# Optimization experiments

Hardware: AMD Instinct MI355X
Metric: run time of the kernel (lower is better)

Reference implementation:

```python
import jax, jax.numpy as jnp
import numpy as np

B = 64; H = 56; W = 56; C = 96; WS = 7; SHIFT = 3; NH = 3
N = WS * WS          # 49 tokens per window
NW = (H // WS) * (W // WS)  # 64 windows per image
HD = C // NH
MLP_H = 4 * C


def _rel_index():
    coords = np.stack(np.meshgrid(np.arange(WS), np.arange(WS), indexing='ij')).reshape(2, -1)
    rel = (coords[:, :, None] - coords[:, None, :]).transpose(1, 2, 0)
    rel[..., 0] += WS - 1
    rel[..., 1] += WS - 1
    rel[..., 0] *= 2 * WS - 1
    return rel.sum(-1)  # [N, N] int


def _attn_mask():
    img = np.zeros((H, W))
    cnt = 0
    sls = (slice(0, -WS), slice(-WS, -SHIFT), slice(-SHIFT, None))
    for hs in sls:
        for ws_ in sls:
            img[hs, ws_] = cnt
            cnt += 1
    mw = img.reshape(H // WS, WS, W // WS, WS).transpose(0, 2, 1, 3).reshape(-1, N)
    diff = mw[:, None, :] - mw[:, :, None]
    return np.where(diff != 0, -100.0, 0.0).astype(np.float32)  # [NW, N, N]


REL_IDX = jnp.asarray(_rel_index())
MASK = jnp.asarray(_attn_mask())


def _ln(x, g, b):
    mu = x.mean(-1, keepdims=True)
    var = ((x - mu) ** 2).mean(-1, keepdims=True)
    return (x - mu) * jax.lax.rsqrt(var + 1e-5) * g + b


def setup_inputs() -> dict:
    key = jax.random.key(0)
    ks = jax.random.split(key, 8)
    s = 0.02
    return {
        'x': jax.random.normal(ks[0], (B, H * W, C), jnp.float32),
        'norm1_g': jnp.ones((C,), jnp.float32),
        'norm1_b': jnp.zeros((C,), jnp.float32),
        'qkv_w': jax.random.normal(ks[1], (C, 3 * C), jnp.float32) * s,
        'qkv_b': jnp.zeros((3 * C,), jnp.float32),
        'proj_w': jax.random.normal(ks[2], (C, C), jnp.float32) * s,
        'proj_b': jnp.zeros((C,), jnp.float32),
        'rpb_table': jax.random.normal(ks[3], ((2 * WS - 1) ** 2, NH), jnp.float32) * s,
        'norm2_g': jnp.ones((C,), jnp.float32),
        'norm2_b': jnp.zeros((C,), jnp.float32),
        'fc1_w': jax.random.normal(ks[4], (C, MLP_H), jnp.float32) * s,
        'fc1_b': jnp.zeros((MLP_H,), jnp.float32),
        'fc2_w': jax.random.normal(ks[5], (MLP_H, C), jnp.float32) * s,
        'fc2_b': jnp.zeros((C,), jnp.float32),
    }


def reference(x, norm1_g, norm1_b, qkv_w, qkv_b, proj_w, proj_b, rpb_table,
              norm2_g, norm2_b, fc1_w, fc1_b, fc2_w, fc2_b):
    Bx = x.shape[0]
    shortcut = x
    h = _ln(x, norm1_g, norm1_b).reshape(Bx, H, W, C)
    # cyclic shift
    h = jnp.roll(h, (-SHIFT, -SHIFT), axis=(1, 2))
    # window partition -> [B*NW, N, C]
    win = h.reshape(Bx, H // WS, WS, W // WS, WS, C).transpose(0, 1, 3, 2, 4, 5).reshape(-1, N, C)
    B_ = win.shape[0]
    # qkv projection
    qkv = (win @ qkv_w + qkv_b).reshape(B_, N, 3, NH, HD).transpose(2, 0, 3, 1, 4)
    q, k, v = qkv[0], qkv[1], qkv[2]  # [B_, NH, N, HD]
    scale = HD ** -0.5
    attn = jnp.einsum('bhnd,bhmd->bhnm', q * scale, k)  # [B_, NH, N, N]
    bias = rpb_table[REL_IDX.reshape(-1)].reshape(N, N, NH).transpose(2, 0, 1)
    attn = attn + bias[None]
    # shifted-window mask
    attn = attn.reshape(Bx, NW, NH, N, N) + MASK[None, :, None]
    attn = jax.nn.softmax(attn.reshape(B_, NH, N, N), axis=-1)
    out = jnp.einsum('bhnm,bhmd->bnhd', attn, v).reshape(B_, N, C)
    out = out @ proj_w + proj_b
    # window reverse + reverse shift
    out = out.reshape(Bx, H // WS, W // WS, WS, WS, C).transpose(0, 1, 3, 2, 4, 5).reshape(Bx, H, W, C)
    out = jnp.roll(out, (SHIFT, SHIFT), axis=(1, 2)).reshape(Bx, H * W, C)
    x = shortcut + out
    # MLP
    h2 = _ln(x, norm2_g, norm2_b)
    h2 = jax.nn.gelu(h2 @ fc1_w + fc1_b, approximate=False) @ fc2_w + fc2_b
    return x + h2
```

## Files before the change

### kernel.cpp

```cpp
#include <hip/hip_runtime.h>
#include <hip/hip_bf16.h>
#include <math.h>

#define BB    64
#define HH    56
#define WW_   56
#define CC    96
#define WS    7
#define SHIFT 3
#define NHD   3
#define NT    49
#define NWIN  64
#define HD    32
#define MLPH  384
#define HWTOK (HH*WW_)
#define NTOK  (BB*HWTOK)
#define NWTOT (BB*NWIN)

#define IMG_S 10240
#define N_IMG 12
#define WS_NEED (16 + N_IMG*IMG_S*2)

typedef __attribute__((ext_vector_type(8))) short short8;
typedef __attribute__((ext_vector_type(4))) short short4v;
typedef __attribute__((ext_vector_type(4))) float floatx4;

__device__ __forceinline__ float b2fs(short s) {
    union { unsigned int u; float f; } cv;
    cv.u = ((unsigned int)(unsigned short)s) << 16;
    return cv.f;
}
__device__ __forceinline__ short f2b(float f) {
    union { __hip_bfloat16 h; short s; } cv;
    cv.h = __float2bfloat16(f);
    return cv.s;
}
__device__ __forceinline__ float ldv(const void* p, size_t i, bool bf) {
    return bf ? b2fs(((const short*)p)[i]) : ((const float*)p)[i];
}
__device__ __forceinline__ void stv(void* p, size_t i, bool bf, float v) {
    if (bf) ((short*)p)[i] = f2b(v);
    else    ((float*)p)[i] = v;
}
#define MFMA16(a,b,c) __builtin_amdgcn_mfma_f32_16x16x32_bf16((a),(b),(c),0,0,0)

__device__ __forceinline__ float gelu_f(float v) {
    float z  = v * 0.70710678118654752f;
    float az = fabsf(z);
    float t  = __fdividef(1.0f, fmaf(0.3275911f, az, 1.0f));
    float p  = fmaf(fmaf(fmaf(fmaf(1.061405429f, t, -1.453152027f), t,
                   1.421413741f), t, -0.284496736f), t, 0.254829592f) * t;
    float e  = __expf(-az*az);
    float er = fmaf(-p, e, 1.0f);
    er = (z < 0.f) ? -er : er;
    return 0.5f * v * (1.0f + er);
}

__global__ void dtype_probe(const void* __restrict__ n1g, int* __restrict__ flag) {
    if (threadIdx.x == 0) {
        float f = ((const float*)n1g)[0];
        *flag = (f == 1.0f) ? 0 : 1;
    }
}

__global__ void prep_kernel(
    const void* __restrict__ qkv_w, const void* __restrict__ proj_w,
    const void* __restrict__ fc1_w, const void* __restrict__ fc2_w,
    short* __restrict__ wimg, const int* __restrict__ flag)
{
    const bool bf = (*flag != 0);
    int idx = blockIdx.x * 256 + threadIdx.x;
    if (idx >= N_IMG*IMG_S) return;
    int img = idx / IMG_S, r = idx - img*IMG_S;
    short v = 0;
    if (r < 96*104) {
        int nc = r / 104, k = r - nc*104;
        if (k < 96) {
            float f;
            if (img < 3)       f = ldv(qkv_w, (size_t)k*(3*CC) + (nc>>5)*CC + img*HD + (nc&31), bf);
            else if (img == 3) f = ldv(proj_w, (size_t)k*CC + nc, bf);
            else if (img < 8)  f = ldv(fc1_w, (size_t)k*MLPH + (img-4)*96 + nc, bf);
            else               f = ldv(fc2_w, (size_t)((img-8)*96 + k)*CC + nc, bf);
            v = f2b(f);
        }
    }
    wimg[idx] = v;
}

__global__ __launch_bounds__(256, 4) void attn_pre2(
    const void* __restrict__ x,
    const void* __restrict__ n1g, const void* __restrict__ n1b,
    const void* __restrict__ qkv_b, const void* __restrict__ rpb,
    const void* __restrict__ proj_b,
    void* __restrict__ out, const int* __restrict__ flag,
    const short* __restrict__ wimg)
{
    __shared__ __attribute__((aligned(16))) short lx[64*104];
    __shared__ __attribute__((aligned(16))) short lqk[64*72];
    __shared__ __attribute__((aligned(16))) short lv[32*72];
    __shared__ __attribute__((aligned(16))) short lsm[64*72];
    __shared__ float lmu[64], lrs[64];
    __shared__ float lg[CC], lb[CC];
    short* lctx = lx;

    const bool bf = (*flag != 0);
    const int win = blockIdx.x;
    const int b   = win >> 6;
    const int wr  = win & 63;
    const int wh  = wr >> 3, ww = wr & 7;
    const int tid = threadIdx.x;
    const int lane = tid & 63;
    const int wv  = tid >> 6;
    const int c   = lane & 15;
    const int q   = lane >> 4;

    if (tid < CC) { lg[tid] = ldv(n1g, tid, bf); lb[tid] = ldv(n1b, tid, bf); }

    if (!bf) {
        const float* xf = (const float*)x;
        for (int idx = tid; idx < NT*24; idx += 256) {
            int n = idx / 24, c4 = idx - n*24;
            int i = n / WS, j = n - i*WS;
            int hg = wh*WS + i + SHIFT; if (hg >= HH)  hg -= HH;
            int wg = ww*WS + j + SHIFT; if (wg >= WW_) wg -= WW_;
            size_t t = (size_t)(b*HWTOK + hg*WW_ + wg);
            floatx4 v = *(const floatx4*)&xf[t*CC + c4*4];
            short4v s;
            s[0] = f2b(v[0]); s[1] = f2b(v[1]); s[2] = f2b(v[2]); s[3] = f2b(v[3]);
            *(short4v*)&lx[n*104 + c4*4] = s;
        }
    } else {
        for (int idx = tid; idx < NT*CC; idx += 256) {
            int n = idx / CC, cc_ = idx - n*CC;
            int i = n / WS, j = n - i*WS;
            int hg = wh*WS + i + SHIFT; if (hg >= HH)  hg -= HH;
            int wg = ww*WS + j + SHIFT; if (wg >= WW_) wg -= WW_;
            size_t t = (size_t)(b*HWTOK + hg*WW_ + wg);
            lx[n*104 + cc_] = f2b(ldv(x, t*CC + cc_, bf));
        }
    }
    for (int idx = tid; idx < 15*13; idx += 256) {
        int n = NT + idx/13, c8 = idx - (idx/13)*13;
        *(short8*)&lx[n*104 + c8*8] = (short8)0;
    }
    __syncthreads();

    {
        int t = tid >> 2, p = tid & 3;
        float s = 0.f, ss = 0.f;
        #pragma unroll
        for (int i = 0; i < 24; ++i) {
            float v = b2fs(lx[t*104 + p*24 + i]); s += v; ss += v*v;
        }
        s += __shfl_xor(s, 1); ss += __shfl_xor(ss, 1);
        s += __shfl_xor(s, 2); ss += __shfl_xor(ss, 2);
        if (p == 0) {
            float mu = s * (1.f/CC);
            float var = ss * (1.f/CC) - mu*mu;
            lmu[t] = mu; lrs[t] = rsqrtf(var + 1e-5f);
        }
    }
    __syncthreads();

    short8 af[3];
    #pragma unroll
    for (int kt = 0; kt < 3; ++kt) {
        int row = wv*16 + c;
        short8 raw = *(const short8*)&lx[row*104 + kt*32 + q*8];
        float mu = lmu[row], rs = lrs[row];
        short8 a;
        #pragma unroll
        for (int e = 0; e < 8; ++e) {
            int k = kt*32 + q*8 + e;
            a[e] = f2b((b2fs(raw[e]) - mu)*rs*lg[k] + lb[k]);
        }
        af[kt] = a;
    }

    const float scale = 0.17677669529663687f;

    for (int h = 0; h < NHD; ++h) {
        const short* bimg = wimg + h*IMG_S;

        floatx4 acc[6];
        #pragma unroll
        for (int nt = 0; nt < 6; ++nt) acc[nt] = (floatx4)0.f;
        #pragma unroll
        for (int kt = 0; kt < 3; ++kt) {
            #pragma unroll
            for (int nt = 0; nt < 6; ++nt) {
                short8 bfr = *(const short8*)&bimg[(nt*16 + c)*104 + kt*32 + q*8];
                acc[nt] = MFMA16(af[kt], bfr, acc[nt]);
            }
        }
        #pragma unroll
        for (int nt = 0; nt < 6; ++nt) {
            int ncol = nt*16 + c;
            int part = ncol >> 5, d = ncol & 31;
            float bias = ldv(qkv_b, part*CC + h*HD + d, bf);
            #pragma unroll
            for (int r = 0; r < 4; ++r) {
                int trow = wv*16 + q*4 + r;
                float v = acc[nt][r] + bias;
                if (part < 2) lqk[trow*72 + part*32 + d] = f2b(v);
                else          lv[d*72 + trow]            = f2b(v);
            }
        }
        __syncthreads();

        short8 aq = *(const short8*)&lqk[(wv*16 + c)*72 + q*8];
        floatx4 sv[4];
        #pragma unroll
        for (int nt = 0; nt < 4; ++nt) {
            short8 bk = *(const short8*)&lqk[(nt*16 + c)*72 + 32 + q*8];
            sv[nt] = MFMA16(aq, bk, (floatx4)0.f);
        }

        int ikA[4], jkA[4], rkA[4], tkA[4];
        #pragma unroll
        for (int nt = 0; nt < 4; ++nt) {
            int tk = nt*16 + c; tkA[nt] = tk;
            int ik = tk / 7, jk = tk - ik*7;
            ikA[nt] = ik; jkA[nt] = jk;
            int rh = (wh == 7) ? (ik < 4 ? 1 : 2) : 0;
            int rw = (ww == 7) ? (jk < 4 ? 1 : 2) : 0;
            rkA[nt] = rh*3 + rw;
        }
        #pragma unroll
        for (int r = 0; r < 4; ++r) {
            int tq = wv*16 + q*4 + r;
            int iq = tq / 7, jq = tq - iq*7;
            int rhq = (wh == 7) ? (iq < 4 ? 1 : 2) : 0;
            int rwq = (ww == 7) ? (jq < 4 ? 1 : 2) : 0;
            int rq = rhq*3 + rwq;
            float vals[4], mx = -1e30f;
            #pragma unroll
            for (int nt = 0; nt < 4; ++nt) {
                float v;
                if (tkA[nt] < NT) {
                    int rel = (iq - ikA[nt] + 6)*13 + (jq - jkA[nt] + 6);
                    rel = rel < 0 ? 0 : (rel > 168 ? 168 : rel);
                    v = sv[nt][r]*scale + ldv(rpb, rel*NHD + h, bf);
                    if (rkA[nt] != rq) v -= 100.f;
                } else v = -1e30f;
                vals[nt] = v; mx = fmaxf(mx, v);
            }
            mx = fmaxf(mx, __shfl_xor(mx, 1));
            mx = fmaxf(mx, __shfl_xor(mx, 2));
            mx = fmaxf(mx, __shfl_xor(mx, 4));
            mx = fmaxf(mx, __shfl_xor(mx, 8));
            float sum = 0.f;
            #pragma unroll
            for (int nt = 0; nt < 4; ++nt) { vals[nt] = __expf(vals[nt] - mx); sum += vals[nt]; }
            sum += __shfl_xor(sum, 1);
            sum += __shfl_xor(sum, 2);
            sum += __shfl_xor(sum, 4);
            sum += __shfl_xor(sum, 8);
            float inv = 1.f / sum;
            #pragma unroll
            for (int nt = 0; nt < 4; ++nt)
                lsm[(wv*16 + q*4 + r)*72 + nt*16 + c] = f2b(vals[nt]*inv);
        }
        floatx4 ov[2] = {(floatx4)0.f, (floatx4)0.f};
        #pragma unroll
        for (int kt = 0; kt < 2; ++kt) {
            short8 ap = *(const short8*)&lsm[(wv*16 + c)*72 + kt*32 + q*8];
            #pragma unroll
            for (int nt = 0; nt < 2; ++nt) {
                short8 bv = *(const short8*)&lv[(nt*16 + c)*72 + kt*32 + q*8];
                ov[nt] = MFMA16(ap, bv, ov[nt]);
            }
        }
        #pragma unroll
        for (int nt = 0; nt < 2; ++nt)
            #pragma unroll
            for (int r = 0; r < 4; ++r)
                lctx[(wv*16 + q*4 + r)*104 + h*HD + nt*16 + c] = f2b(ov[nt][r]);
        if (h < NHD-1) __syncthreads();
    }

    const short* pimg = wimg + 3*IMG_S;
    floatx4 po[6];
    #pragma unroll
    for (int nt = 0; nt < 6; ++nt) po[nt] = (floatx4)0.f;
    #pragma unroll
    for (int kt = 0; kt < 3; ++kt) {
        short8 ac = *(const short8*)&lctx[(wv*16 + c)*104 + kt*32 + q*8];
        #pragma unroll
        for (int nt = 0; nt < 6; ++nt) {
            short8 bp = *(const short8*)&pimg[(nt*16 + c)*104 + kt*32 + q*8];
            po[nt] = MFMA16(ac, bp, po[nt]);
        }
    }
    float pbv[6];
    #pragma unroll
    for (int nt = 0; nt < 6; ++nt) pbv[nt] = ldv(proj_b, nt*16 + c, bf);
    #pragma unroll
    for (int r = 0; r < 4; ++r) {
        int n = wv*16 + q*4 + r;
        if (n < NT) {
            int i = n / WS, j = n - i*WS;
            int hg = wh*WS + i + SHIFT; if (hg >= HH)  hg -= HH;
            int wg = ww*WS + j + SHIFT; if (wg >= WW_) wg -= WW_;
            size_t gbase = (size_t)(b*HWTOK + hg*WW_ + wg)*CC;
            #pragma unroll
            for (int nt = 0; nt < 6; ++nt) {
                size_t gi = gbase + nt*16 + c;
                stv(out, gi, bf, po[nt][r] + pbv[nt] + ldv(x, gi, bf));
            }
        }
    }
}

__global__ __launch_bounds__(256, 2) void mlp_x2(
    void* __restrict__ out,
    const void* __restrict__ n2g, const void* __restrict__ n2b,
    const void* __restrict__ fc1_b, const void* __restrict__ fc2_b,
    const int* __restrict__ flag, const short* __restrict__ wimg)
{
    __shared__ __attribute__((aligned(16))) short lx1[128*104];
    __shared__ float lmu[128], lrs[128];
    __shared__ float lg[CC], lb[CC];
    short* lh = lx1;

    const bool bf = (*flag != 0);
    const int t0  = blockIdx.x * 128;
    const int tid = threadIdx.x;
    const int lane = tid & 63;
    const int wv  = tid >> 6;
    const int rb  = wv * 32;
    const int c   = lane & 15;
    const int q   = lane >> 4;

    if (tid < CC) { lg[tid] = ldv(n2g, tid, bf); lb[tid] = ldv(n2b, tid, bf); }

    if (!bf) {
        const float* of = (const float*)out;
        for (int idx = lane; idx < 32*24; idx += 64) {
            int n = idx / 24, c4 = idx - n*24;
            floatx4 v = *(const floatx4*)&of[(size_t)(t0+rb+n)*CC + c4*4];
            short4v s;
            s[0] = f2b(v[0]); s[1] = f2b(v[1]); s[2] = f2b(v[2]); s[3] = f2b(v[3]);
            *(short4v*)&lx1[(rb+n)*104 + c4*4] = s;
        }
    } else {
        for (int idx = lane; idx < 32*CC; idx += 64) {
            int n = idx / CC, cc_ = idx - n*CC;
            lx1[(rb+n)*104 + cc_] = f2b(ldv(out, (size_t)(t0+rb+n)*CC + cc_, bf));
        }
    }

    {
        int tr = rb + (lane >> 1), p = lane & 1;
        float s = 0.f, ss = 0.f;
        #pragma unroll
        for (int i = 0; i < 48; ++i) {
            float v = b2fs(lx1[tr*104 + p*48 + i]); s += v; ss += v*v;
        }
        s += __shfl_xor(s, 1); ss += __shfl_xor(ss, 1);
        if (p == 0) {
            float mu = s * (1.f/CC);
            float var = ss * (1.f/CC) - mu*mu;
            lmu[tr] = mu; lrs[tr] = rsqrtf(var + 1e-5f);
        }
    }
    __syncthreads();

    short8 af[2][3];
    #pragma unroll
    for (int tt = 0; tt < 2; ++tt) {
        #pragma unroll
        for (int kt = 0; kt < 3; ++kt) {
            int row = rb + tt*16 + c;
            short8 raw = *(const short8*)&lx1[row*104 + kt*32 + q*8];
            float mu = lmu[row], rs = lrs[row];
            short8 a;
            #pragma unroll
            for (int e = 0; e < 8; ++e) {
                int k = kt*32 + q*8 + e;
                a[e] = f2b((b2fs(raw[e]) - mu)*rs*lg[k] + lb[k]);
            }
            af[tt][kt] = a;
        }
    }

    floatx4 acc2[2][6];
    #pragma unroll
    for (int tt = 0; tt < 2; ++tt)
        #pragma unroll
        for (int nt = 0; nt < 6; ++nt) acc2[tt][nt] = (floatx4)0.f;

    for (int qh = 0; qh < 4; ++qh) {
        const short* b1 = wimg + (4+qh)*IMG_S;
        #pragma unroll
        for (int nh = 0; nh < 2; ++nh) {
            floatx4 a1[2][3];
            #pragma unroll
            for (int tt = 0; tt < 2; ++tt)
                #pragma unroll
                for (int nt2 = 0; nt2 < 3; ++nt2) a1[tt][nt2] = (floatx4)0.f;
            #pragma unroll
            for (int kt = 0; kt < 3; ++kt) {
                #pragma unroll
                for (int nt2 = 0; nt2 < 3; ++nt2) {
                    int nt = nh*3 + nt2;
                    short8 bfr = *(const short8*)&b1[(nt*16 + c)*104 + kt*32 + q*8];
                    a1[0][nt2] = MFMA16(af[0][kt], bfr, a1[0][nt2]);
                    a1[1][nt2] = MFMA16(af[1][kt], bfr, a1[1][nt2]);
                }
            }
            #pragma unroll
            for (int nt2 = 0; nt2 < 3; ++nt2) {
                int nl = (nh*3 + nt2)*16 + c;
                float bias = ldv(fc1_b, qh*96 + nl, bf);
                #pragma unroll
                for (int tt = 0; tt < 2; ++tt) {
                    #pragma unroll
                    for (int r = 0; r < 4; ++r) {
                        float v = a1[tt][nt2][r] + bias;
                        lh[(rb + tt*16 + q*4 + r)*104 + nl] = f2b(gelu_f(v));
                    }
                }
            }
        }
        __syncthreads();

        const short* b2 = wimg + (8+qh)*IMG_S;
        #pragma unroll
        for (int kt = 0; kt < 3; ++kt) {
            short8 ah0 = *(const short8*)&lh[(rb + c)*104 + kt*32 + q*8];
            short8 ah1 = *(const short8*)&lh[(rb + 16 + c)*104 + kt*32 + q*8];
            #pragma unroll
            for (int nt = 0; nt < 6; ++nt) {
                short8 bw = *(const short8*)&b2[(nt*16 + c)*104 + kt*32 + q*8];
                acc2[0][nt] = MFMA16(ah0, bw, acc2[0][nt]);
                acc2[1][nt] = MFMA16(ah1, bw, acc2[1][nt]);
            }
        }
    }

    float b2v[6];
    #pragma unroll
    for (int nt = 0; nt < 6; ++nt) b2v[nt] = ldv(fc2_b, nt*16 + c, bf);
    #pragma unroll
    for (int tt = 0; tt < 2; ++tt) {
        #pragma unroll
        for (int r = 0; r < 4; ++r) {
            int row = rb + tt*16 + q*4 + r;
            size_t gbase = (size_t)(t0 + row)*CC;
            #pragma unroll
            for (int nt = 0; nt < 6; ++nt) {
                size_t gi = gbase + nt*16 + c;
                stv(out, gi, bf, acc2[tt][nt][r] + b2v[nt] + ldv(out, gi, bf));
            }
        }
    }
}

__global__ __launch_bounds__(256, 2) void attn_old(
    const void* __restrict__ x,
    const void* __restrict__ n1g, const void* __restrict__ n1b,
    const void* __restrict__ qkv_w, const void* __restrict__ qkv_b,
    const void* __restrict__ rpb,
    const void* __restrict__ proj_w, const void* __restrict__ proj_b,
    void* __restrict__ out, const int* __restrict__ flag)
{
    __shared__ __attribute__((aligned(16))) short lx[64*104];
    __shared__ __attribute__((aligned(16))) short lwb[96*104];
    __shared__ __attribute__((aligned(16))) short lqk[64*72];
    __shared__ __attribute__((aligned(16))) short lv[32*72];
    __shared__ __attribute__((aligned(16))) short lctx[64*104];
    __shared__ float lmu[64], lrs[64];
    __shared__ float lg[CC], lb[CC];
    short* lsm = lwb;

    const bool bf = (*flag != 0);
    const int win = blockIdx.x;
    const int b   = win >> 6;
    const int wr  = win & 63;
    const int wh  = wr >> 3, ww = wr & 7;
    const int tid = threadIdx.x;
    const int lane = tid & 63;
    const int wv  = tid >> 6;
    const int c   = lane & 15;
    const int q   = lane >> 4;

    if (tid < CC) { lg[tid] = ldv(n1g, tid, bf); lb[tid] = ldv(n1b, tid, bf); }

    for (int idx = tid; idx < NT*CC; idx += 256) {
        int n = idx / CC, cc_ = idx - n*CC;
        int i = n / WS, j = n - i*WS;
        int hg = wh*WS + i + SHIFT; if (hg >= HH)  hg -= HH;
        int wg = ww*WS + j + SHIFT; if (wg >= WW_) wg -= WW_;
        size_t t = (size_t)(b*HWTOK + hg*WW_ + wg);
        lx[n*104 + cc_] = f2b(ldv(x, t*CC + cc_, bf));
    }
    for (int idx = tid; idx < 15*CC; idx += 256) {
        int n = NT + idx/CC, cc_ = idx % CC;
        lx[n*104 + cc_] = 0;
    }
    __syncthreads();

    {
        int t = tid >> 2, p = tid & 3;
        float s = 0.f, ss = 0.f;
        #pragma unroll
        for (int i = 0; i < 24; ++i) {
            float v = b2fs(lx[t*104 + p*24 + i]); s += v; ss += v*v;
        }
        s += __shfl_xor(s, 1); ss += __shfl_xor(ss, 1);
        s += __shfl_xor(s, 2); ss += __shfl_xor(ss, 2);
        if (p == 0) {
            float mu = s * (1.f/CC);
            float var = ss * (1.f/CC) - mu*mu;
            lmu[t] = mu; lrs[t] = rsqrtf(var + 1e-5f);
        }
    }
    __syncthreads();
    for (int idx = tid; idx < NT*CC; idx += 256) {
        int n = idx / CC, cc_ = idx - n*CC;
        float v = b2fs(lx[n*104 + cc_]);
        lx[n*104 + cc_] = f2b((v - lmu[n]) * lrs[n] * lg[cc_] + lb[cc_]);
    }
    __syncthreads();

    const float scale = 0.17677669529663687f;

    for (int h = 0; h < NHD; ++h) {
        for (int idx = tid; idx < 96*96; idx += 256) {
            int k = idx / 96, nc = idx - (idx/96)*96;
            int part = nc >> 5, d = nc & 31;
            lwb[nc*104 + k] = f2b(ldv(qkv_w, (size_t)k*(3*CC) + part*CC + h*HD + d, bf));
        }
        __syncthreads();

        floatx4 acc[6];
        #pragma unroll
        for (int nt = 0; nt < 6; ++nt) acc[nt] = (floatx4)0.f;
        #pragma unroll
        for (int kt = 0; kt < 3; ++kt) {
            short8 af = *(const short8*)&lx[(wv*16 + c)*104 + kt*32 + q*8];
            #pragma unroll
            for (int nt = 0; nt < 6; ++nt) {
                short8 bfr = *(const short8*)&lwb[(nt*16 + c)*104 + kt*32 + q*8];
                acc[nt] = MFMA16(af, bfr, acc[nt]);
            }
        }
        #pragma unroll
        for (int nt = 0; nt < 6; ++nt) {
            int ncol = nt*16 + c;
            int part = ncol >> 5, d = ncol & 31;
            float bias = ldv(qkv_b, part*CC + h*HD + d, bf);
            #pragma unroll
            for (int r = 0; r < 4; ++r) {
                int trow = wv*16 + q*4 + r;
                float v = acc[nt][r] + bias;
                if (part < 2) lqk[trow*72 + part*32 + d] = f2b(v);
                else          lv[d*72 + trow]            = f2b(v);
            }
        }
        __syncthreads();

        short8 aq = *(const short8*)&lqk[(wv*16 + c)*72 + q*8];
        floatx4 sv[4];
        #pragma unroll
        for (int nt = 0; nt < 4; ++nt) {
            short8 bk = *(const short8*)&lqk[(nt*16 + c)*72 + 32 + q*8];
            sv[nt] = MFMA16(aq, bk, (floatx4)0.f);
        }

        int ikA[4], jkA[4], rkA[4], tkA[4];
        #pragma unroll
        for (int nt = 0; nt < 4; ++nt) {
            int tk = nt*16 + c; tkA[nt] = tk;
            int ik = tk / 7, jk = tk - ik*7;
            ikA[nt] = ik; jkA[nt] = jk;
            int rh = (wh == 7) ? (ik < 4 ? 1 : 2) : 0;
            int rw = (ww == 7) ? (jk < 4 ? 1 : 2) : 0;
            rkA[nt] = rh*3 + rw;
        }
        #pragma unroll
        for (int r = 0; r < 4; ++r) {
            int tq = wv*16 + q*4 + r;
            int iq = tq / 7, jq = tq - iq*7;
            int rhq = (wh == 7) ? (iq < 4 ? 1 : 2) : 0;
            int rwq = (ww == 7) ? (jq < 4 ? 1 : 2) : 0;
            int rq = rhq*3 + rwq;
            float vals[4], mx = -1e30f;
            #pragma unroll
            for (int nt = 0; nt < 4; ++nt) {
                float v;
                if (tkA[nt] < NT) {
                    int rel = (iq - ikA[nt] + 6)*13 + (jq - jkA[nt] + 6);
                    rel = rel < 0 ? 0 : (rel > 168 ? 168 : rel);
                    v = sv[nt][r]*scale + ldv(rpb, rel*NHD + h, bf);
                    if (rkA[nt] != rq) v -= 100.f;
                } else v = -1e30f;
                vals[nt] = v; mx = fmaxf(mx, v);
            }
            mx = fmaxf(mx, __shfl_xor(mx, 1));
            mx = fmaxf(mx, __shfl_xor(mx, 2));
            mx = fmaxf(mx, __shfl_xor(mx, 4));
            mx = fmaxf(mx, __shfl_xor(mx, 8));
            float sum = 0.f;
            #pragma unroll
            for (int nt = 0; nt < 4; ++nt) { vals[nt] = __expf(vals[nt] - mx); sum += vals[nt]; }
            sum += __shfl_xor(sum, 1);
            sum += __shfl_xor(sum, 2);
            sum += __shfl_xor(sum, 4);
            sum += __shfl_xor(sum, 8);
            float inv = 1.f / sum;
            #pragma unroll
            for (int nt = 0; nt < 4; ++nt)
                lsm[(wv*16 + q*4 + r)*72 + nt*16 + c] = f2b(vals[nt]*inv);
        }
        floatx4 ov[2] = {(floatx4)0.f, (floatx4)0.f};
        #pragma unroll
        for (int kt = 0; kt < 2; ++kt) {
            short8 ap = *(const short8*)&lsm[(wv*16 + c)*72 + kt*32 + q*8];
            #pragma unroll
            for (int nt = 0; nt < 2; ++nt) {
                short8 bv = *(const short8*)&lv[(nt*16 + c)*72 + kt*32 + q*8];
                ov[nt] = MFMA16(ap, bv, ov[nt]);
            }
        }
        #pragma unroll
        for (int nt = 0; nt < 2; ++nt)
            #pragma unroll
            for (int r = 0; r < 4; ++r)
                lctx[(wv*16 + q*4 + r)*104 + h*HD + nt*16 + c] = f2b(ov[nt][r]);
        __syncthreads();
    }

    for (int idx = tid; idx < 96*96; idx += 256) {
        int k = idx / 96, nc = idx - (idx/96)*96;
        lwb[nc*104 + k] = f2b(ldv(proj_w, (size_t)k*CC + nc, bf));
    }
    __syncthreads();

    floatx4 po[6];
    #pragma unroll
    for (int nt = 0; nt < 6; ++nt) po[nt] = (floatx4)0.f;
    #pragma unroll
    for (int kt = 0; kt < 3; ++kt) {
        short8 ac = *(const short8*)&lctx[(wv*16 + c)*104 + kt*32 + q*8];
        #pragma unroll
        for (int nt = 0; nt < 6; ++nt) {
            short8 bp = *(const short8*)&lwb[(nt*16 + c)*104 + kt*32 + q*8];
            po[nt] = MFMA16(ac, bp, po[nt]);
        }
    }
    #pragma unroll
    for (int nt = 0; nt < 6; ++nt) {
        int ncol = nt*16 + c;
        float bias = ldv(proj_b, ncol, bf);
        #pragma unroll
        for (int r = 0; r < 4; ++r) {
            int n = wv*16 + q*4 + r;
            if (n < NT) {
                int i = n / WS, j = n - i*WS;
                int hg = wh*WS + i + SHIFT; if (hg >= HH)  hg -= HH;
                int wg = ww*WS + j + SHIFT; if (wg >= WW_) wg -= WW_;
                size_t t = (size_t)(b*HWTOK + hg*WW_ + wg);
                stv(out, t*CC + ncol, bf, po[nt][r] + bias + ldv(x, t*CC + ncol, bf));
            }
        }
    }
}

__global__ __launch_bounds__(256, 3) void mlp_old(
    void* __restrict__ out,
    const void* __restrict__ n2g, const void* __restrict__ n2b,
    const void* __restrict__ fc1_w, const void* __restrict__ fc1_b,
    const void* __restrict__ fc2_w, const void* __restrict__ fc2_b,
    const int* __restrict__ flag)
{
    __shared__ __attribute__((aligned(16))) short lx1[64*104];
    __shared__ __attribute__((aligned(16))) short lh[64*104];
    __shared__ __attribute__((aligned(16))) short lw[96*104];
    __shared__ float lmu[64], lrs[64];
    __shared__ float lg[CC], lb[CC];

    const bool bf = (*flag != 0);
    const int t0  = blockIdx.x * 64;
    const int tid = threadIdx.x;
    const int lane = tid & 63;
    const int wv  = tid >> 6;
    const int c   = lane & 15;
    const int q   = lane >> 4;

    if (tid < CC) { lg[tid] = ldv(n2g, tid, bf); lb[tid] = ldv(n2b, tid, bf); }
    for (int idx = tid; idx < 64*CC; idx += 256) {
        int n = idx / CC, cc_ = idx - n*CC;
        lx1[n*104 + cc_] = f2b(ldv(out, (size_t)(t0+n)*CC + cc_, bf));
    }
    __syncthreads();

    {
        int t = tid >> 2, p = tid & 3;
        float s = 0.f, ss = 0.f;
        #pragma unroll
        for (int i = 0; i < 24; ++i) {
            float v = b2fs(lx1[t*104 + p*24 + i]); s += v; ss += v*v;
        }
        s += __shfl_xor(s, 1); ss += __shfl_xor(ss, 1);
        s += __shfl_xor(s, 2); ss += __shfl_xor(ss, 2);
        if (p == 0) {
            float mu = s * (1.f/CC);
            float var = ss * (1.f/CC) - mu*mu;
            lmu[t] = mu; lrs[t] = rsqrtf(var + 1e-5f);
        }
    }
    __syncthreads();

    short8 af[3];
    #pragma unroll
    for (int kt = 0; kt < 3; ++kt) {
        int row = wv*16 + c;
        short8 raw = *(const short8*)&lx1[row*104 + kt*32 + q*8];
        float mu = lmu[row], rs = lrs[row];
        short8 a;
        #pragma unroll
        for (int e = 0; e < 8; ++e) {
            int k = kt*32 + q*8 + e;
            a[e] = f2b((b2fs(raw[e]) - mu)*rs*lg[k] + lb[k]);
        }
        af[kt] = a;
    }

    floatx4 acc2[6];
    #pragma unroll
    for (int nt = 0; nt < 6; ++nt) acc2[nt] = (floatx4)0.f;

    for (int qh = 0; qh < 4; ++qh) {
        for (int idx = tid; idx < 96*96; idx += 256) {
            int k = idx / 96, nl = idx - (idx/96)*96;
            lw[nl*104 + k] = f2b(ldv(fc1_w, (size_t)k*MLPH + qh*96 + nl, bf));
        }
        __syncthreads();

        floatx4 a1[6];
        #pragma unroll
        for (int nt = 0; nt < 6; ++nt) a1[nt] = (floatx4)0.f;
        #pragma unroll
        for (int kt = 0; kt < 3; ++kt) {
            #pragma unroll
            for (int nt = 0; nt < 6; ++nt) {
                short8 bfr = *(const short8*)&lw[(nt*16 + c)*104 + kt*32 + q*8];
                a1[nt] = MFMA16(af[kt], bfr, a1[nt]);
            }
        }
        #pragma unroll
        for (int nt = 0; nt < 6; ++nt) {
            int nl = nt*16 + c;
            float bias = ldv(fc1_b, qh*96 + nl, bf);
            #pragma unroll
            for (int r = 0; r < 4; ++r) {
                float v = a1[nt][r] + bias;
                float g = 0.5f*v*(1.f + erff(v*0.70710678118654752f));
                lh[(wv*16 + q*4 + r)*104 + nl] = f2b(g);
            }
        }
        __syncthreads();

        for (int idx = tid; idx < 96*96; idx += 256) {
            int kl = idx / 96, n = idx - (idx/96)*96;
            lw[n*104 + kl] = f2b(ldv(fc2_w, (size_t)(qh*96 + kl)*CC + n, bf));
        }
        __syncthreads();

        #pragma unroll
        for (int kt = 0; kt < 3; ++kt) {
            short8 ah = *(const short8*)&lh[(wv*16 + c)*104 + kt*32 + q*8];
            #pragma unroll
            for (int nt = 0; nt < 6; ++nt) {
                short8 bw = *(const short8*)&lw[(nt*16 + c)*104 + kt*32 + q*8];
                acc2[nt] = MFMA16(ah, bw, acc2[nt]);
            }
        }
        __syncthreads();
    }

    #pragma unroll
    for (int nt = 0; nt < 6; ++nt) {
        int ncol = nt*16 + c;
        float bias = ldv(fc2_b, ncol, bf);
        #pragma unroll
        for (int r = 0; r < 4; ++r) {
            int row = wv*16 + q*4 + r;
            size_t gi = (size_t)(t0 + row)*CC + ncol;
            stv(out, gi, bf, acc2[nt][r] + bias + ldv(out, gi, bf));
        }
    }
}

__global__ void mfma_probe(void* __restrict__ out, const int* __restrict__ flag) {
    __shared__ float A[16*32];
    __shared__ float Bm[32*16];
    __shared__ __attribute__((aligned(16))) short As[16*104];
    __shared__ int lf1[64], lf2[64];

    const bool bfm = (*flag != 0);
    const int tid = threadIdx.x;
    for (int i = tid; i < 16*32; i += 64) {
        int m = i >> 5, k = i & 31;
        A[i] = (float)((m*7 + k*3) % 11 - 5) * 0.125f;
    }
    for (int i = tid; i < 32*16; i += 64) {
        int k = i >> 4, n = i & 15;
        Bm[i] = (float)((k*5 + n*2) % 13 - 6) * 0.0625f;
    }
    __syncthreads();
    for (int i = tid; i < 16*32; i += 64) {
        int m = i >> 5, k = i & 31;
        As[m*104 + k] = f2b(A[i]);
    }
    __syncthreads();

    const int c = tid & 15, q = tid >> 4;
    short8 a, b;
    #pragma unroll
    for (int j = 0; j < 8; ++j) {
        a[j] = f2b(A[c*32 + q*8 + j]);
        b[j] = f2b(Bm[(q*8 + j)*16 + c]);
    }
    short8 av = *(const short8*)&As[c*104 + q*8];
    int f2 = 0;
    #pragma unroll
    for (int j = 0; j < 8; ++j) if (av[j] != a[j]) f2 = 1;

    floatx4 acc = (floatx4)0.f;
    acc = MFMA16(a, b, acc);
    int f1 = 0;
    #pragma unroll
    for (int r = 0; r < 4; ++r) {
        float ref = 0.f;
        for (int k = 0; k < 32; ++k)
            ref += b2fs(f2b(A[(q*4 + r)*32 + k])) * b2fs(f2b(Bm[k*16 + c]));
        float d = fabsf(acc[r] - ref);
        if (!(d <= 0.02f)) f1 = 1;
    }
    lf1[tid] = f1; lf2[tid] = f2;
    __syncthreads();

    if (tid == 0) {
        int any1 = 0, any2 = 0;
        for (int i = 0; i < 64; ++i) { any1 |= lf1[i]; any2 |= lf2[i]; }
        float pert = any1 ? 0.06f : 0.f;
        float tiny = 0.f;
        if (any2) {
            float s = 1.0001f;
            for (int i = 0; i < 400000; ++i) s = s * 0.9999999f + 1e-9f;
            tiny = s * 1e-38f;
        }
        stv(out, 0, bfm, ldv(out, 0, bfm) + pert + tiny);
    }
}

extern "C" void kernel_launch(void* const* d_in, const int* in_sizes, int n_in,
                              void* d_out, int out_size, void* d_ws, size_t ws_size,
                              hipStream_t stream) {
    const void* x      = d_in[0];
    const void* n1g    = d_in[1];
    const void* n1b    = d_in[2];
    const void* qkv_w  = d_in[3];
    const void* qkv_b  = d_in[4];
    const void* proj_w = d_in[5];
    const void* proj_b = d_in[6];
    const void* rpb    = d_in[7];
    const void* n2g    = d_in[8];
    const void* n2b    = d_in[9];
    const void* fc1_w  = d_in[10];
    const void* fc1_b  = d_in[11];
    const void* fc2_w  = d_in[12];
    const void* fc2_b  = d_in[13];
    int* flag = (int*)d_ws;

    hipLaunchKernelGGL(dtype_probe, dim3(1), dim3(64), 0, stream, n1g, flag);

    if (ws_size >= (size_t)WS_NEED) {
        short* wimg = (short*)((char*)d_ws + 16);
        hipLaunchKernelGGL(prep_kernel, dim3((N_IMG*IMG_S + 255)/256), dim3(256), 0, stream,
                           qkv_w, proj_w, fc1_w, fc2_w, wimg, flag);
        hipLaunchKernelGGL(attn_pre2, dim3(NWTOT), dim3(256), 0, stream,
                           x, n1g, n1b, qkv_b, rpb, proj_b, d_out, flag, wimg);
        hipLaunchKernelGGL(mlp_x2, dim3(NTOK/128), dim3(256), 0, stream,
                           d_out, n2g, n2b, fc1_b, fc2_b, flag, wimg);
    } else {
        hipLaunchKernelGGL(attn_old, dim3(NWTOT), dim3(256), 0, stream,
                           x, n1g, n1b, qkv_w, qkv_b, rpb, proj_w, proj_b, d_out, flag);
        hipLaunchKernelGGL(mlp_old, dim3(NTOK/64), dim3(256), 0, stream,
                           d_out, n2g, n2b, fc1_w, fc1_b, fc2_w, fc2_b, flag);
    }
    hipLaunchKernelGGL(mfma_probe, dim3(1), dim3(64), 0, stream, d_out, flag);
}
```

Measured before the change: 489.3 us.

## Process each attention window with two waves, each covering 32 rows

The window attention kernel now runs 128 threads (two waves) per window instead of four, with each wave handling two 16-row tiles. B-fragments loaded from the weight image are shared across the two tiles, and per-wave copies of the LayerNorm parameters plus wave-local row ownership remove two block barriers. The softmax buffer is aliased onto the QK buffer, with an added barrier, to cut LDS use. The aim is less redundant weight loading and fewer syncs, at the cost of more registers per thread and possibly less latency hiding per window.

```diff
diff --git a/kernel.cpp b/kernel.cpp
--- a/kernel.cpp
+++ b/kernel.cpp
@@ -87,7 +87,7 @@
     wimg[idx] = v;
 }
 
-__global__ __launch_bounds__(256, 4) void attn_pre2(
+__global__ __launch_bounds__(128, 2) void attn_x2(
     const void* __restrict__ x,
     const void* __restrict__ n1g, const void* __restrict__ n1b,
     const void* __restrict__ qkv_b, const void* __restrict__ rpb,
@@ -98,10 +98,10 @@
     __shared__ __attribute__((aligned(16))) short lx[64*104];
     __shared__ __attribute__((aligned(16))) short lqk[64*72];
     __shared__ __attribute__((aligned(16))) short lv[32*72];
-    __shared__ __attribute__((aligned(16))) short lsm[64*72];
     __shared__ float lmu[64], lrs[64];
-    __shared__ float lg[CC], lb[CC];
+    __shared__ float lgw[2][CC], lbw[2][CC];
     short* lctx = lx;
+    short* lsm  = lqk;
 
     const bool bf = (*flag != 0);
     const int win = blockIdx.x;
@@ -110,16 +110,23 @@
     const int wh  = wr >> 3, ww = wr & 7;
     const int tid = threadIdx.x;
     const int lane = tid & 63;
-    const int wv  = tid >> 6;
+    const int w   = tid >> 6;
+    const int rb  = w * 32;
     const int c   = lane & 15;
     const int q   = lane >> 4;
 
-    if (tid < CC) { lg[tid] = ldv(n1g, tid, bf); lb[tid] = ldv(n1b, tid, bf); }
-
+    lgw[w][lane] = ldv(n1g, lane, bf);
+    lbw[w][lane] = ldv(n1b, lane, bf);
+    if (lane < CC-64) {
+        lgw[w][64+lane] = ldv(n1g, 64+lane, bf);
+        lbw[w][64+lane] = ldv(n1b, 64+lane, bf);
+    }
+
+    const int rows = (w == 0) ? 32 : (NT - 32);
     if (!bf) {
         const float* xf = (const float*)x;
-        for (int idx = tid; idx < NT*24; idx += 256) {
-            int n = idx / 24, c4 = idx - n*24;
+        for (int idx = lane; idx < rows*24; idx += 64) {
+            int n = rb + idx/24, c4 = idx - (idx/24)*24;
             int i = n / WS, j = n - i*WS;
             int hg = wh*WS + i + SHIFT; if (hg >= HH)  hg -= HH;
             int wg = ww*WS + j + SHIFT; if (wg >= WW_) wg -= WW_;
@@ -130,8 +137,8 @@
             *(short4v*)&lx[n*104 + c4*4] = s;
         }
     } else {
-        for (int idx = tid; idx < NT*CC; idx += 256) {
-            int n = idx / CC, cc_ = idx - n*CC;
+        for (int idx = lane; idx < rows*CC; idx += 64) {
+            int n = rb + idx/CC, cc_ = idx - (idx/CC)*CC;
             int i = n / WS, j = n - i*WS;
             int hg = wh*WS + i + SHIFT; if (hg >= HH)  hg -= HH;
             int wg = ww*WS + j + SHIFT; if (wg >= WW_) wg -= WW_;
@@ -139,42 +146,44 @@
             lx[n*104 + cc_] = f2b(ldv(x, t*CC + cc_, bf));
         }
     }
-    for (int idx = tid; idx < 15*13; idx += 256) {
-        int n = NT + idx/13, c8 = idx - (idx/13)*13;
-        *(short8*)&lx[n*104 + c8*8] = (short8)0;
-    }
-    __syncthreads();
+    if (w == 1) {
+        for (int idx = lane; idx < 15*13; idx += 64) {
+            int n = NT + idx/13, c8 = idx - (idx/13)*13;
+            *(short8*)&lx[n*104 + c8*8] = (short8)0;
+        }
+    }
 
     {
-        int t = tid >> 2, p = tid & 3;
+        int tr = rb + (lane >> 1), p = lane & 1;
         float s = 0.f, ss = 0.f;
         #pragma unroll
-        for (int i = 0; i < 24; ++i) {
-            float v = b2fs(lx[t*104 + p*24 + i]); s += v; ss += v*v;
+        for (int i = 0; i < 48; ++i) {
+            float v = b2fs(lx[tr*104 + p*48 + i]); s += v; ss += v*v;
         }
         s += __shfl_xor(s, 1); ss += __shfl_xor(ss, 1);
-        s += __shfl_xor(s, 2); ss += __shfl_xor(ss, 2);
         if (p == 0) {
             float mu = s * (1.f/CC);
             float var = ss * (1.f/CC) - mu*mu;
-            lmu[t] = mu; lrs[t] = rsqrtf(var + 1e-5f);
-        }
-    }
-    __syncthreads();
-
-    short8 af[3];
-    #pragma unroll
-    for (int kt = 0; kt < 3; ++kt) {
-        int row = wv*16 + c;
-        short8 raw = *(const short8*)&lx[row*104 + kt*32 + q*8];
-        float mu = lmu[row], rs = lrs[row];
-        short8 a;
-        #pragma unroll
-        for (int e = 0; e < 8; ++e) {
-            int k = kt*32 + q*8 + e;
-            a[e] = f2b((b2fs(raw[e]) - mu)*rs*lg[k] + lb[k]);
-        }
-        af[kt] = a;
+            lmu[tr] = mu; lrs[tr] = rsqrtf(var + 1e-5f);
+        }
+    }
+
+    short8 af[2][3];
+    #pragma unroll
+    for (int tt = 0; tt < 2; ++tt) {
+        #pragma unroll
+        for (int kt = 0; kt < 3; ++kt) {
+            int row = rb + tt*16 + c;
+            short8 raw = *(const short8*)&lx[row*104 + kt*32 + q*8];
+            float mu = lmu[row], rs = lrs[row];
+            short8 a;
+            #pragma unroll
+            for (int e = 0; e < 8; ++e) {
+                int k = kt*32 + q*8 + e;
+                a[e] = f2b((b2fs(raw[e]) - mu)*rs*lgw[w][k] + lbw[w][k]);
+            }
+            af[tt][kt] = a;
+        }
     }
 
     const float scale = 0.17677669529663687f;
@@ -182,15 +191,18 @@
     for (int h = 0; h < NHD; ++h) {
         const short* bimg = wimg + h*IMG_S;
 
-        floatx4 acc[6];
-        #pragma unroll
-        for (int nt = 0; nt < 6; ++nt) acc[nt] = (floatx4)0.f;
+        floatx4 acc[2][6];
+        #pragma unroll
+        for (int tt = 0; tt < 2; ++tt)
+            #pragma unroll
+            for (int nt = 0; nt < 6; ++nt) acc[tt][nt] = (floatx4)0.f;
         #pragma unroll
         for (int kt = 0; kt < 3; ++kt) {
             #pragma unroll
             for (int nt = 0; nt < 6; ++nt) {
                 short8 bfr = *(const short8*)&bimg[(nt*16 + c)*104 + kt*32 + q*8];
-                acc[nt] = MFMA16(af[kt], bfr, acc[nt]);
+                acc[0][nt] = MFMA16(af[0][kt], bfr, acc[0][nt]);
+                acc[1][nt] = MFMA16(af[1][kt], bfr, acc[1][nt]);
             }
         }
         #pragma unroll
@@ -199,22 +211,28 @@
             int part = ncol >> 5, d = ncol & 31;
             float bias = ldv(qkv_b, part*CC + h*HD + d, bf);
             #pragma unroll
-            for (int r = 0; r < 4; ++r) {
-                int trow = wv*16 + q*4 + r;
-                float v = acc[nt][r] + bias;
-                if (part < 2) lqk[trow*72 + part*32 + d] = f2b(v);
-                else          lv[d*72 + trow]            = f2b(v);
+            for (int tt = 0; tt < 2; ++tt) {
+                #pragma unroll
+                for (int r = 0; r < 4; ++r) {
+                    int trow = rb + tt*16 + q*4 + r;
+                    float v = acc[tt][nt][r] + bias;
+                    if (part < 2) lqk[trow*72 + part*32 + d] = f2b(v);
+                    else          lv[d*72 + trow]            = f2b(v);
+                }
             }
         }
         __syncthreads();
 
-        short8 aq = *(const short8*)&lqk[(wv*16 + c)*72 + q*8];
-        floatx4 sv[4];
+        short8 aq0 = *(const short8*)&lqk[(rb + c)*72 + q*8];
+        short8 aq1 = *(const short8*)&lqk[(rb + 16 + c)*72 + q*8];
+        floatx4 sv[2][4];
         #pragma unroll
         for (int nt = 0; nt < 4; ++nt) {
             short8 bk = *(const short8*)&lqk[(nt*16 + c)*72 + 32 + q*8];
-            sv[nt] = MFMA16(aq, bk, (floatx4)0.f);
-        }
+            sv[0][nt] = MFMA16(aq0, bk, (floatx4)0.f);
+            sv[1][nt] = MFMA16(aq1, bk, (floatx4)0.f);
+        }
+        __syncthreads();
 
         int ikA[4], jkA[4], rkA[4], tkA[4];
         #pragma unroll
@@ -227,86 +245,102 @@
             rkA[nt] = rh*3 + rw;
         }
         #pragma unroll
-        for (int r = 0; r < 4; ++r) {
-            int tq = wv*16 + q*4 + r;
-            int iq = tq / 7, jq = tq - iq*7;
-            int rhq = (wh == 7) ? (iq < 4 ? 1 : 2) : 0;
-            int rwq = (ww == 7) ? (jq < 4 ? 1 : 2) : 0;
-            int rq = rhq*3 + rwq;
-            float vals[4], mx = -1e30f;
-            #pragma unroll
-            for (int nt = 0; nt < 4; ++nt) {
-                float v;
-                if (tkA[nt] < NT) {
-                    int rel = (iq - ikA[nt] + 6)*13 + (jq - jkA[nt] + 6);
-                    rel = rel < 0 ? 0 : (rel > 168 ? 168 : rel);
-                    v = sv[nt][r]*scale + ldv(rpb, rel*NHD + h, bf);
-                    if (rkA[nt] != rq) v -= 100.f;
-                } else v = -1e30f;
-                vals[nt] = v; mx = fmaxf(mx, v);
-            }
-            mx = fmaxf(mx, __shfl_xor(mx, 1));
-            mx = fmaxf(mx, __shfl_xor(mx, 2));
-            mx = fmaxf(mx, __shfl_xor(mx, 4));
-            mx = fmaxf(mx, __shfl_xor(mx, 8));
-            float sum = 0.f;
-            #pragma unroll
-            for (int nt = 0; nt < 4; ++nt) { vals[nt] = __expf(vals[nt] - mx); sum += vals[nt]; }
-            sum += __shfl_xor(sum, 1);
-            sum += __shfl_xor(sum, 2);
-            sum += __shfl_xor(sum, 4);
-            sum += __shfl_xor(sum, 8);
-            float inv = 1.f / sum;
-            #pragma unroll
-            for (int nt = 0; nt < 4; ++nt)
-                lsm[(wv*16 + q*4 + r)*72 + nt*16 + c] = f2b(vals[nt]*inv);
-        }
-        floatx4 ov[2] = {(floatx4)0.f, (floatx4)0.f};
+        for (int tt = 0; tt < 2; ++tt) {
+            #pragma unroll
+            for (int r = 0; r < 4; ++r) {
+                int tq = rb + tt*16 + q*4 + r;
+                int iq = tq / 7, jq = tq - iq*7;
+                int rhq = (wh == 7) ? (iq < 4 ? 1 : 2) : 0;
+                int rwq = (ww == 7) ? (jq < 4 ? 1 : 2) : 0;
+                int rq = rhq*3 + rwq;
+                float vals[4], mx = -1e30f;
+                #pragma unroll
+                for (int nt = 0; nt < 4; ++nt) {
+                    float v;
+                    if (tkA[nt] < NT) {
+                        int rel = (iq - ikA[nt] + 6)*13 + (jq - jkA[nt] + 6);
+                        rel = rel < 0 ? 0 : (rel > 168 ? 168 : rel);
+                        v = sv[tt][nt][r]*scale + ldv(rpb, rel*NHD + h, bf);
+                        if (rkA[nt] != rq) v -= 100.f;
+                    } else v = -1e30f;
+                    vals[nt] = v; mx = fmaxf(mx, v);
+                }
+                mx = fmaxf(mx, __shfl_xor(mx, 1));
+                mx = fmaxf(mx, __shfl_xor(mx, 2));
+                mx = fmaxf(mx, __shfl_xor(mx, 4));
+                mx = fmaxf(mx, __shfl_xor(mx, 8));
+                float sum = 0.f;
+                #pragma unroll
+                for (int nt = 0; nt < 4; ++nt) { vals[nt] = __expf(vals[nt] - mx); sum += vals[nt]; }
+                sum += __shfl_xor(sum, 1);
+                sum += __shfl_xor(sum, 2);
+                sum += __shfl_xor(sum, 4);
+                sum += __shfl_xor(sum, 8);
+                float inv = 1.f / sum;
+                #pragma unroll
+                for (int nt = 0; nt < 4; ++nt)
+                    lsm[tq*72 + nt*16 + c] = f2b(vals[nt]*inv);
+            }
+        }
+        floatx4 ov[2][2];
+        ov[0][0] = (floatx4)0.f; ov[0][1] = (floatx4)0.f;
+        ov[1][0] = (floatx4)0.f; ov[1][1] = (floatx4)0.f;
         #pragma unroll
         for (int kt = 0; kt < 2; ++kt) {
-            short8 ap = *(const short8*)&lsm[(wv*16 + c)*72 + kt*32 + q*8];
+            short8 ap0 = *(const short8*)&lsm[(rb + c)*72 + kt*32 + q*8];
+            short8 ap1 = *(const short8*)&lsm[(rb + 16 + c)*72 + kt*32 + q*8];
             #pragma unroll
             for (int nt = 0; nt < 2; ++nt) {
                 short8 bv = *(const short8*)&lv[(nt*16 + c)*72 + kt*32 + q*8];
-                ov[nt] = MFMA16(ap, bv, ov[nt]);
-            }
-        }
-        #pragma unroll
-        for (int nt = 0; nt < 2; ++nt)
-            #pragma unroll
-            for (int r = 0; r < 4; ++r)
-                lctx[(wv*16 + q*4 + r)*104 + h*HD + nt*16 + c] = f2b(ov[nt][r]);
+                ov[0][nt] = MFMA16(ap0, bv, ov[0][nt]);
+                ov[1][nt] = MFMA16(ap1, bv, ov[1][nt]);
+            }
+        }
+        #pragma unroll
+        for (int tt = 0; tt < 2; ++tt)
+            #pragma unroll
+            for (int nt = 0; nt < 2; ++nt)
+                #pragma unroll
+                for (int r = 0; r < 4; ++r)
+                    lctx[(rb + tt*16 + q*4 + r)*104 + h*HD + nt*16 + c] = f2b(ov[tt][nt][r]);
         if (h < NHD-1) __syncthreads();
     }
 
     const short* pimg = wimg + 3*IMG_S;
-    floatx4 po[6];
-    #pragma unroll
-    for (int nt = 0; nt < 6; ++nt) po[nt] = (floatx4)0.f;
+    floatx4 po[2][6];
+    #pragma unroll
+    for (int tt = 0; tt < 2; ++tt)
+        #pragma unroll
+        for (int nt = 0; nt < 6; ++nt) po[tt][nt] = (floatx4)0.f;
     #pragma unroll
     for (int kt = 0; kt < 3; ++kt) {
-        short8 ac = *(const short8*)&lctx[(wv*16 + c)*104 + kt*32 + q*8];
+        short8 ac0 = *(const short8*)&lctx[(rb + c)*104 + kt*32 + q*8];
+        short8 ac1 = *(const short8*)&lctx[(rb + 16 + c)*104 + kt*32 + q*8];
         #pragma unroll
         for (int nt = 0; nt < 6; ++nt) {
             short8 bp = *(const short8*)&pimg[(nt*16 + c)*104 + kt*32 + q*8];
-            po[nt] = MFMA16(ac, bp, po[nt]);
+            po[0][nt] = MFMA16(ac0, bp, po[0][nt]);
+            po[1][nt] = MFMA16(ac1, bp, po[1][nt]);
         }
     }
     float pbv[6];
     #pragma unroll
     for (int nt = 0; nt < 6; ++nt) pbv[nt] = ldv(proj_b, nt*16 + c, bf);
     #pragma unroll
-    for (int r = 0; r < 4; ++r) {
-        int n = wv*16 + q*4 + r;
-        if (n < NT) {
-            int i = n / WS, j = n - i*WS;
-            int hg = wh*WS + i + SHIFT; if (hg >= HH)  hg -= HH;
-            int wg = ww*WS + j + SHIFT; if (wg >= WW_) wg -= WW_;
-            size_t gbase = (size_t)(b*HWTOK + hg*WW_ + wg)*CC;
-            #pragma unroll
-            for (int nt = 0; nt < 6; ++nt) {
-                size_t gi = gbase + nt*16 + c;
-                stv(out, gi, bf, po[nt][r] + pbv[nt] + ldv(x, gi, bf));
+    for (int tt = 0; tt < 2; ++tt) {
+        #pragma unroll
+        for (int r = 0; r < 4; ++r) {
+            int n = rb + tt*16 + q*4 + r;
+            if (n < NT) {
+                int i = n / WS, j = n - i*WS;
+                int hg = wh*WS + i + SHIFT; if (hg >= HH)  hg -= HH;
+                int wg = ww*WS + j + SHIFT; if (wg >= WW_) wg -= WW_;
+                size_t gbase = (size_t)(b*HWTOK + hg*WW_ + wg)*CC;
+                #pragma unroll
+                for (int nt = 0; nt < 6; ++nt) {
+                    size_t gi = gbase + nt*16 + c;
+                    stv(out, gi, bf, po[tt][nt][r] + pbv[nt] + ldv(x, gi, bf));
+                }
             }
         }
     }
@@ -882,7 +916,7 @@
         short* wimg = (short*)((char*)d_ws + 16);
         hipLaunchKernelGGL(prep_kernel, dim3((N_IMG*IMG_S + 255)/256), dim3(256), 0, stream,
                            qkv_w, proj_w, fc1_w, fc2_w, wimg, flag);
-        hipLaunchKernelGGL(attn_pre2, dim3(NWTOT), dim3(256), 0, stream,
+        hipLaunchKernelGGL(attn_x2, dim3(NWTOT), dim3(128), 0, stream,
                            x, n1g, n1b, qkv_b, rpb, proj_b, d_out, flag, wimg);
         hipLaunchKernelGGL(mlp_x2, dim3(NTOK/128), dim3(256), 0, stream,
                            d_out, n2g, n2b, fc1_b, fc2_b, flag, wimg);
```

Measured after the change: 541.1 us. 1.11x slower.
